# Kernel tuning notes

Measured on AMD Instinct MI355X. Metric: run time of the kernel, lower is better.

The kernel has to match this reference:

```python
import jax, jax.numpy as jnp
import numpy as np

N_HEADS = 16
LN_EPS = 1e-5

def layer_norm(x, w):
    # matches torch LayerNorm in fp32, weight-only (no bias)
    x = x.astype(jnp.float32)
    mu = jnp.mean(x, axis=-1, keepdims=True)
    var = jnp.mean((x - mu) ** 2, axis=-1, keepdims=True)
    return (x - mu) / jnp.sqrt(var + LN_EPS) * w

def rotate_half(t):
    t1, t2 = jnp.split(t, 2, axis=-1)
    return jnp.concatenate((-t2, t1), axis=-1)

def setup_inputs() -> dict:
    key = jax.random.key(0)
    ks = jax.random.split(key, 16)
    B, S, D, C = 2, 2048, 1024, 1024
    H = N_HEADS
    hd = D // H
    # rotary tables: emb = cat(freqs, freqs), freqs = t * inv_freq
    inv_freq = 1.0 / (10000.0 ** (np.arange(0, hd, 2, dtype=np.float32) / hd))
    t = np.arange(S, dtype=np.float32)
    freqs = np.outer(t, inv_freq)                       # [S, hd/2]
    emb = np.concatenate([freqs, freqs], axis=-1)       # [S, hd]
    s = 0.02
    return {
        "x": jax.random.normal(ks[0], (B, S, D), jnp.float32),
        "rotary_cos": jnp.asarray(np.cos(emb)),
        "rotary_sin": jnp.asarray(np.sin(emb)),
        "c": jax.random.normal(ks[1], (B, C), jnp.float32),
        "norm1_w": jnp.ones((D,), jnp.float32),
        "qkv_w": jax.random.normal(ks[2], (3 * D, D), jnp.float32) * s,
        "out_w": jax.random.normal(ks[3], (D, D), jnp.float32) * s,
        "norm2_w": jnp.ones((D,), jnp.float32),
        "fc1_w": jax.random.normal(ks[4], (4 * D, D), jnp.float32) * s,
        "fc1_b": jnp.zeros((4 * D,), jnp.float32),
        "fc2_w": jax.random.normal(ks[5], (D, 4 * D), jnp.float32) * s,
        "fc2_b": jnp.zeros((D,), jnp.float32),
        # NOTE: module zero-inits adaLN; random here for a non-degenerate baseline
        "ada_w": jax.random.normal(ks[6], (6 * D, C), jnp.float32) * s,
        "ada_b": jnp.zeros((6 * D,), jnp.float32),
    }

def reference(x, rotary_cos, rotary_sin, c, norm1_w, qkv_w, out_w, norm2_w,
              fc1_w, fc1_b, fc2_w, fc2_b, ada_w, ada_b):
    B, S, D = x.shape
    H = N_HEADS
    hd = D // H
    # AdaLN conditioning -> six [B,1,D] modulation tensors
    mods = (c @ ada_w.T + ada_b)[:, None, :]                       # [B,1,6D]
    shift_msa, scale_msa, gate_msa, shift_mlp, scale_mlp, gate_mlp = jnp.split(mods, 6, axis=2)
    x_skip = x
    # LN + modulate + QKV
    h = layer_norm(x, norm1_w) * (1.0 + scale_msa) + shift_msa     # [B,S,D]
    qkv = (h @ qkv_w.T).reshape(B, S, 3, H, hd)
    # rotary applied to packed qkv (q, k, and v) as in the torchscript fallback
    cos = rotary_cos[None, :, None, None, :]                       # [1,S,1,1,hd]
    sin = rotary_sin[None, :, None, None, :]
    qkv = qkv * cos + rotate_half(qkv) * sin
    q, k, v = qkv[:, :, 0], qkv[:, :, 1], qkv[:, :, 2]             # [B,S,H,hd]
    scale = hd ** -0.5
    scores = jnp.einsum('bqhd,bkhd->bhqk', q, k) * scale           # [B,H,S,S]
    attn = jax.nn.softmax(scores, axis=-1)
    o = jnp.einsum('bhqk,bkhd->bqhd', attn, v).reshape(B, S, D)
    # gated residual (dropout=0 / eval)
    x = gate_msa * (o @ out_w.T) + x_skip
    # second LN + modulate + MLP (exact gelu, matching F.gelu default)
    h2 = layer_norm(x, norm2_w) * (1.0 + scale_mlp) + shift_mlp
    mlp = jax.nn.gelu(h2 @ fc1_w.T + fc1_b, approximate=False) @ fc2_w.T + fc2_b
    return gate_mlp * mlp + x
```

## Files before the change

kernel.cpp:

```cpp
#include <hip/hip_runtime.h>
#include <hip/hip_bf16.h>


typedef unsigned short u16;
typedef unsigned int   u32;
typedef __bf16 bf16x8 __attribute__((ext_vector_type(8)));
typedef float  f32x4  __attribute__((ext_vector_type(4)));

#define MFMA_BF16(a, b, c) __builtin_amdgcn_mfma_f32_16x16x32_bf16((a), (b), (c), 0, 0, 0)

__device__ __forceinline__ float b2f(u16 u) {
    union { u32 i; float f; } v; v.i = ((u32)u) << 16; return v.f;
}
__device__ __forceinline__ u16 f2b(float f) {
    union { u32 i; float f; } v; v.f = f;
    u32 i = v.i;
    return (u16)((i + 0x7FFFu + ((i >> 16) & 1u)) >> 16);
}
__device__ __forceinline__ u32 pk2(float a, float b) {
#if __has_builtin(__builtin_amdgcn_cvt_pk_bf16_f32)
    typedef __bf16 bf16x2_t __attribute__((ext_vector_type(2)));
    union { bf16x2_t v; u32 u; } cv;
    cv.v = __builtin_amdgcn_cvt_pk_bf16_f32(a, b);
    return cv.u;
#else
    return (u32)f2b(a) | ((u32)f2b(b) << 16);
#endif
}
__device__ __forceinline__ float exp2_raw(float x) {
#if __has_builtin(__builtin_amdgcn_exp2f)
    return __builtin_amdgcn_exp2f(x);
#else
    float r;
    __asm("v_exp_f32 %0, %1" : "=v"(r) : "v"(x));
    return r;
#endif
}
__device__ __forceinline__ float finz(float v) {
    return __builtin_isfinite(v) ? v : 0.0f;
}
__device__ __forceinline__ void dma16(const void* g, void* l) {
    __builtin_amdgcn_global_load_lds(
        (const __attribute__((address_space(1))) unsigned int*)(uintptr_t)g,
        (__attribute__((address_space(3))) unsigned int*)(uintptr_t)l,
        16, 0, 0);
}

__global__ __launch_bounds__(256) void convert_kernel(
    const float* __restrict__ in, u16* __restrict__ out, int n8, int kshift)
{
    int i = blockIdx.x * 256 + threadIdx.x;
    if (i >= n8) return;
    size_t o = (size_t)i * 8;
    int bk   = (int)(o >> (kshift + 7));
    int rem  = (int)(o & (((size_t)128 << kshift) - 1));
    int kg   = rem >> 10;
    int nloc = (rem >> 3) & 127;
    const float* src = in + (((size_t)bk * 128 + nloc) << kshift) + kg * 8;
    float4 a = *(const float4*)src;
    float4 b = *(const float4*)(src + 4);
    union { u16 s[8]; float4 v; } wp;
    wp.s[0] = f2b(a.x); wp.s[1] = f2b(a.y); wp.s[2] = f2b(a.z); wp.s[3] = f2b(a.w);
    wp.s[4] = f2b(b.x); wp.s[5] = f2b(b.y); wp.s[6] = f2b(b.z); wp.s[7] = f2b(b.w);
    *(float4*)(out + o) = wp.v;
}

__global__ __launch_bounds__(64) void mods_kernel(
    const float* __restrict__ c, const float* __restrict__ ada_w,
    const float* __restrict__ ada_b, float* __restrict__ mods)
{
    const int n = blockIdx.x;
    const int lane = threadIdx.x;
    const float* wr = ada_w + (size_t)n * 1024;
    float a0 = 0.f, a1 = 0.f;
    for (int k = lane; k < 1024; k += 64) {
        float w = wr[k];
        a0 += w * c[k];
        a1 += w * c[1024 + k];
    }
    for (int o = 32; o > 0; o >>= 1) {
        a0 += __shfl_down(a0, o, 64);
        a1 += __shfl_down(a1, o, 64);
    }
    if (lane == 0) {
        float bb = ada_b[n];
        mods[n]        = a0 + bb;
        mods[6144 + n] = a1 + bb;
    }
}

__global__ __launch_bounds__(256) void ln_mod_kernel(
    const u16* __restrict__ xbf, const float* __restrict__ xf,
    const float* __restrict__ w, const float* __restrict__ mods,
    int scale_off, int shift_off, u16* __restrict__ out)
{
    const int row = blockIdx.x;
    const int b   = row >> 11;
    const int tid = threadIdx.x;
    const int wave = tid >> 6, lane = tid & 63;
    const size_t base = (size_t)row * 1024 + tid * 4;
    float v[4];
    if (xf) {
        float4 t = *(const float4*)(xf + base);
        v[0] = t.x; v[1] = t.y; v[2] = t.z; v[3] = t.w;
    } else {
        uint2 p = *(const uint2*)(xbf + base);
        union { u32 i; float f; } a, bb, cc, d;
        a.i  = p.x << 16;          v[0] = a.f;
        bb.i = p.x & 0xFFFF0000u;  v[1] = bb.f;
        cc.i = p.y << 16;          v[2] = cc.f;
        d.i  = p.y & 0xFFFF0000u;  v[3] = d.f;
    }
    float s  = v[0] + v[1] + v[2] + v[3];
    float sq = v[0]*v[0] + v[1]*v[1] + v[2]*v[2] + v[3]*v[3];
    #pragma unroll
    for (int o = 32; o > 0; o >>= 1) {
        s  += __shfl_down(s,  o, 64);
        sq += __shfl_down(sq, o, 64);
    }
    __shared__ float ws[8];
    if (lane == 0) { ws[wave] = s; ws[4 + wave] = sq; }
    __syncthreads();
    const float ts = (ws[0] + ws[1]) + (ws[2] + ws[3]);
    const float tq = (ws[4] + ws[5]) + (ws[6] + ws[7]);
    const float mean = ts * (1.0f / 1024.0f);
    const float var  = tq * (1.0f / 1024.0f) - mean * mean;
    const float inv  = rsqrtf(fmaxf(var, 0.f) + 1e-5f);
    union { u16 s4[4]; uint2 u2; } pk;
    for (int i = 0; i < 4; ++i) {
        int cidx = tid * 4 + i;
        float y = (v[i] - mean) * inv * w[cidx];
        y = y * (1.0f + mods[b * 6144 + scale_off + cidx]) + mods[b * 6144 + shift_off + cidx];
        pk.s4[i] = f2b(y);
    }
    size_t o = ((size_t)(row >> 7)) * 131072 + ((tid * 4) >> 3) * 1024
             + (row & 127) * 8 + ((tid * 4) & 7);
    *(uint2*)(out + o) = pk.u2;
}

template<int MODE, int TM>
__global__ __launch_bounds__(256) void gemm128(
    const u16* __restrict__ A, const u16* __restrict__ W,
    int M, int N, int K,
    const float* __restrict__ mods, const float* __restrict__ bias,
    const float* __restrict__ resid_f, const u16* __restrict__ resid_bf,
    float* __restrict__ out_f, u16* __restrict__ out_bf,
    u16* __restrict__ aux1, u16* __restrict__ aux2,
    const float* __restrict__ rcos, const float* __restrict__ rsin)
{
    constexpr int FI    = TM / 32;
    constexpr int WROWS = TM / 2;
    constexpr int ATILE = TM * 32;
    __shared__ u16 As[3][ATILE];
    __shared__ u16 Bs[3][4096];
    const int tid  = threadIdx.x;
    const int wave = tid >> 6, lane = tid & 63;
    const int quad = lane >> 4, l15 = lane & 15;
    const int wi = wave >> 1, wj = wave & 1;
    const int m0 = blockIdx.y * TM, n0 = blockIdx.x * 128;

    f32x4 acc[FI][4] = {};

    const u16* Asrc = A + (size_t)(m0 >> 7) * 128 * K + (m0 & 127) * 8
                        + wave * 1024 + lane * 8;
    const u16* Bsrc = W + (size_t)n0 * K + wave * 1024 + lane * 8;

    auto stage = [&](int tt, int buf) {
        const u16* a = Asrc + (size_t)tt * 4096;
        const u16* b = Bsrc + (size_t)tt * 4096;
        if constexpr (TM == 128) {
            dma16(a,       &As[buf][wave * 1024]);
            dma16(a + 512, &As[buf][wave * 1024 + 512]);
        } else {
            dma16(a, &As[buf][wave * 512]);
        }
        dma16(b,       &Bs[buf][wave * 1024]);
        dma16(b + 512, &Bs[buf][wave * 1024 + 512]);
    };

    const int nt = K >> 5;
    stage(0, 0);
    stage(1, 1);

    int cur = 0;
    for (int t = 0; t < nt; ++t) {
        if (t + 1 < nt) {
            if constexpr (TM == 128)
                __asm volatile("s_waitcnt vmcnt(4)" ::: "memory");
            else
                __asm volatile("s_waitcnt vmcnt(3)" ::: "memory");
        } else {
            __asm volatile("s_waitcnt vmcnt(0)" ::: "memory");
        }
        __builtin_amdgcn_s_barrier();
        if (t + 2 < nt) {
            int nb = cur + 2; if (nb >= 3) nb -= 3;
            stage(t + 2, nb);
        }
        bf16x8 af[FI], bw[4];
        #pragma unroll
        for (int f = 0; f < FI; ++f)
            af[f] = *(const bf16x8*)(&As[cur][quad * (TM * 8) + (wi * WROWS + f * 16 + l15) * 8]);
        #pragma unroll
        for (int f = 0; f < 4; ++f)
            bw[f] = *(const bf16x8*)(&Bs[cur][quad * 1024 + (wj * 64 + f * 16 + l15) * 8]);
        #pragma unroll
        for (int fi = 0; fi < FI; ++fi)
            #pragma unroll
            for (int fj = 0; fj < 4; ++fj)
                acc[fi][fj] = MFMA_BF16(af[fi], bw[fj], acc[fi][fj]);
        cur = (cur + 1 == 3) ? 0 : cur + 1;
    }

    if (MODE == 4) {
        const int colbase = n0 + wj * 64;
        const int wcol = colbase >> 10;
        const int hh   = (colbase & 1023) >> 6;
        #pragma unroll
        for (int fi = 0; fi < FI; ++fi) {
            const int rbase = m0 + wi * WROWS + fi * 16 + quad * 4;
            #pragma unroll
            for (int reg = 0; reg < 4; ++reg) {
                const int r = rbase + reg;
                const int b = r >> 11, s = r & 2047;
                const int bh = b * 16 + hh;
                #pragma unroll
                for (int fj = 0; fj < 2; ++fj) {
                    const int d2 = fj * 16 + l15;
                    float va = acc[fi][fj][reg];
                    float vb = acc[fi][fj + 2][reg];
                    float ca = rcos[s * 64 + d2];
                    float sa = rsin[s * 64 + d2];
                    float ra = va * ca - vb * sa;
                    float rb = vb * ca + va * sa;
                    if (wcol == 0) {
                        ra *= 0.18033688011f; rb *= 0.18033688011f;
                        u16* dst = aux1 + ((size_t)bh * 2048 + s) * 64;
                        dst[d2]      = f2b(ra);
                        dst[d2 + 32] = f2b(rb);
                    } else if (wcol == 1) {
                        size_t base = (size_t)bh * 131072 + (s >> 6) * 4096
                                    + (s & 63) * 8 + (d2 & 7);
                        aux2[base + (d2 >> 3) * 512]        = f2b(ra);
                        aux2[base + ((d2 >> 3) + 4) * 512]  = f2b(rb);
                    } else {
                        const int sl = s & 63;
                        const int sp = (sl & 32) | ((sl & 15) << 1) | ((sl >> 4) & 1);
                        size_t base = (size_t)bh * 131072 + (s >> 6) * 4096
                                    + (sp >> 3) * 512 + (sp & 7);
                        out_bf[base + d2 * 8]        = f2b(ra);
                        out_bf[base + (d2 + 32) * 8] = f2b(rb);
                    }
                }
            }
        }
        return;
    }

    #pragma unroll
    for (int fi = 0; fi < FI; ++fi) {
        #pragma unroll
        for (int fj = 0; fj < 4; ++fj) {
            const int cidx  = n0 + wj * 64 + fj * 16 + l15;
            const int rbase = m0 + wi * WROWS + fi * 16 + quad * 4;
            #pragma unroll
            for (int reg = 0; reg < 4; ++reg) {
                const int r = rbase + reg;
                float v = acc[fi][fj][reg];
                if (MODE == 1) {
                    float u = v + bias[cidx];
                    float g = 0.5f * u * (1.0f + erff(u * 0.70710678118654752f));
                    size_t o = ((size_t)(r >> 7)) * 524288 + (cidx >> 3) * 1024
                             + (r & 127) * 8 + (cidx & 7);
                    out_bf[o] = f2b(g);
                } else if (MODE == 2) {
                    int bb = r >> 11;
                    float gate = mods[bb * 6144 + 2048 + cidx];
                    out_bf[(size_t)r * N + cidx] = f2b(gate * v + resid_f[(size_t)r * N + cidx]);
                } else if (MODE == 3) {
                    int bb = r >> 11;
                    float u = v + bias[cidx];
                    float gate = mods[bb * 6144 + 5120 + cidx];
                    out_f[(size_t)r * N + cidx] =
                        finz(gate * u + b2f(resid_bf[(size_t)r * N + cidx]));
                }
            }
        }
    }
}

__global__ __launch_bounds__(256, 4) void attn_kernel(
    const u16* __restrict__ Q, const u16* __restrict__ Kb,
    const u16* __restrict__ Vb, u16* __restrict__ O)
{
    __shared__ u16 Ks[4096];
    __shared__ u16 Vs[4096];
    __shared__ u16 Ps[4][16 * 72];
    const int tid  = threadIdx.x;
    const int wave = tid >> 6, lane = tid & 63;
    const int quad = lane >> 4, l15 = lane & 15;
    const int bh = blockIdx.x & 31, qt = blockIdx.x >> 5;

    const u16* Qh = Q + ((size_t)bh * 2048 + qt * 64) * 64;

    const int soff = (2 * wave) * 512 + lane * 8;
    const u16* kSrc = Kb + (size_t)bh * 131072 + soff;
    const u16* vSrc = Vb + (size_t)bh * 131072 + soff;
    u16* kDst0 = &Ks[(2 * wave) * 512];
    u16* kDst1 = &Ks[(2 * wave + 1) * 512];
    u16* vDst0 = &Vs[(2 * wave) * 512];
    u16* vDst1 = &Vs[(2 * wave + 1) * 512];

    bf16x8 aq[2];
    #pragma unroll
    for (int kh = 0; kh < 2; ++kh)
        aq[kh] = *(const bf16x8*)(Qh + (size_t)(wave * 16 + l15) * 64 + kh * 32 + quad * 8);

    f32x4 acc_o[4] = {};
    float lsum[4] = {0.f, 0.f, 0.f, 0.f};

    for (int kb = 0; kb < 32; ++kb) {
        __syncthreads();
        dma16(kSrc,       kDst0);
        dma16(kSrc + 512, kDst1);
        dma16(vSrc,       vDst0);
        dma16(vSrc + 512, vDst1);
        kSrc += 4096; vSrc += 4096;
        __syncthreads();

        f32x4 sc[4] = {};
        #pragma unroll
        for (int kt = 0; kt < 4; ++kt)
            #pragma unroll
            for (int kh = 0; kh < 2; ++kh) {
                bf16x8 bk = *(const bf16x8*)(&Ks[(quad + kh * 4) * 512 + (kt * 16 + l15) * 8]);
                sc[kt] = MFMA_BF16(aq[kh], bk, sc[kt]);
            }

        #pragma unroll
        for (int kt = 0; kt < 4; ++kt)
            #pragma unroll
            for (int reg = 0; reg < 4; ++reg)
                sc[kt][reg] = exp2_raw(fminf(sc[kt][reg], 72.f));
        #pragma unroll
        for (int reg = 0; reg < 4; ++reg)
            lsum[reg] += (sc[0][reg] + sc[1][reg]) + (sc[2][reg] + sc[3][reg]);

        #pragma unroll
        for (int reg = 0; reg < 4; ++reg) {
            u32* prow = (u32*)(&Ps[wave][(quad * 4 + reg) * 72]);
            prow[l15]      = pk2(sc[0][reg], sc[1][reg]);
            prow[16 + l15] = pk2(sc[2][reg], sc[3][reg]);
        }
        __asm volatile("s_waitcnt lgkmcnt(0)" ::: "memory");

        bf16x8 ap0 = *(const bf16x8*)(&Ps[wave][l15 * 72 + quad * 8]);
        bf16x8 ap1 = *(const bf16x8*)(&Ps[wave][l15 * 72 + 32 + quad * 8]);
        #pragma unroll
        for (int dt = 0; dt < 4; ++dt) {
            bf16x8 bv0 = *(const bf16x8*)(&Vs[quad * 512 + (dt * 16 + l15) * 8]);
            bf16x8 bv1 = *(const bf16x8*)(&Vs[(quad + 4) * 512 + (dt * 16 + l15) * 8]);
            acc_o[dt] = MFMA_BF16(ap0, bv0, acc_o[dt]);
            acc_o[dt] = MFMA_BF16(ap1, bv1, acc_o[dt]);
        }
    }

    float linv[4];
    #pragma unroll
    for (int reg = 0; reg < 4; ++reg) {
        float l = lsum[reg];
        l += __shfl_xor(l, 1, 64);
        l += __shfl_xor(l, 2, 64);
        l += __shfl_xor(l, 4, 64);
        l += __shfl_xor(l, 8, 64);
        linv[reg] = 1.0f / l;
    }

    const int b = bh >> 4, hh = bh & 15;
    #pragma unroll
    for (int dt = 0; dt < 4; ++dt)
        #pragma unroll
        for (int reg = 0; reg < 4; ++reg) {
            int q = qt * 64 + wave * 16 + quad * 4 + reg;
            int r = b * 2048 + q;
            int col = hh * 64 + dt * 16 + l15;
            float v = acc_o[dt][reg] * linv[reg];
            O[((size_t)(r >> 7)) * 131072 + (col >> 3) * 1024
              + (r & 127) * 8 + (col & 7)] = f2b(v);
        }
}

extern "C" void kernel_launch(void* const* d_in, const int* in_sizes, int n_in,
                              void* d_out, int out_size, void* d_ws, size_t ws_size,
                              hipStream_t stream)
{
    const float* x     = (const float*)d_in[0];
    const float* rcos  = (const float*)d_in[1];
    const float* rsin  = (const float*)d_in[2];
    const float* c     = (const float*)d_in[3];
    const float* n1w   = (const float*)d_in[4];
    const float* qkvw  = (const float*)d_in[5];
    const float* outw  = (const float*)d_in[6];
    const float* n2w   = (const float*)d_in[7];
    const float* fc1w  = (const float*)d_in[8];
    const float* fc1b  = (const float*)d_in[9];
    const float* fc2w  = (const float*)d_in[10];
    const float* fc2b  = (const float*)d_in[11];
    const float* adaw  = (const float*)d_in[12];
    const float* adab  = (const float*)d_in[13];
    float* out = (float*)d_out;

    char* ws = (char*)d_ws;
    const size_t MB8 = (size_t)8 * 1024 * 1024;
    float* mods  = (float*)ws;
    u16*   W     = (u16*)(ws + 49152);
    char*  S1    = ws + 49152 + MB8;
    char*  S2    = S1 + MB8;

    u16* h    = (u16*)d_out;
    u16* qs   = (u16*)S1;
    u16* ks   = (u16*)S2;
    u16* vT   = (u16*)(S2 + MB8);
    u16* ob   = (u16*)d_out;
    u16* x2   = (u16*)S1;
    u16* h2   = (u16*)d_out;
    u16* mid  = (u16*)S2;

    mods_kernel<<<6144, 64, 0, stream>>>(c, adaw, adab, mods);
    ln_mod_kernel<<<4096, 256, 0, stream>>>(nullptr, x, n1w, mods, 1024, 0, h);
    convert_kernel<<<1536, 256, 0, stream>>>(qkvw, W, 393216, 10);
    gemm128<4, 128><<<dim3(24, 32), 256, 0, stream>>>(h, W, 4096, 3072, 1024,
        nullptr, nullptr, nullptr, nullptr, nullptr, vT, qs, ks, rcos, rsin);
    attn_kernel<<<1024, 256, 0, stream>>>(qs, ks, vT, ob);
    convert_kernel<<<512, 256, 0, stream>>>(outw, W, 131072, 10);
    gemm128<2, 64><<<dim3(8, 64), 256, 0, stream>>>(ob, W, 4096, 1024, 1024,
        mods, nullptr, x, nullptr, nullptr, x2, nullptr, nullptr, nullptr, nullptr);
    ln_mod_kernel<<<4096, 256, 0, stream>>>(x2, nullptr, n2w, mods, 4096, 3072, h2);
    convert_kernel<<<2048, 256, 0, stream>>>(fc1w, W, 524288, 10);
    gemm128<1, 128><<<dim3(32, 32), 256, 0, stream>>>(h2, W, 4096, 4096, 1024,
        nullptr, fc1b, nullptr, nullptr, nullptr, mid, nullptr, nullptr, nullptr, nullptr);
    convert_kernel<<<2048, 256, 0, stream>>>(fc2w, W, 524288, 12);
    gemm128<3, 64><<<dim3(8, 64), 256, 0, stream>>>(mid, W, 4096, 1024, 4096,
        mods, fc2b, nullptr, x2, out, nullptr, nullptr, nullptr, nullptr, nullptr);
}
```

Measured before the change: 384.0 us.

## Double attention query tile to 128 rows and merge QKV/out weight conversions

```diff
diff --git a/kernel.cpp b/kernel.cpp
--- a/kernel.cpp
+++ b/kernel.cpp
@@ -46,11 +46,9 @@
         16, 0, 0);
 }
 
-__global__ __launch_bounds__(256) void convert_kernel(
-    const float* __restrict__ in, u16* __restrict__ out, int n8, int kshift)
-{
-    int i = blockIdx.x * 256 + threadIdx.x;
-    if (i >= n8) return;
+__device__ __forceinline__ void convert_body(
+    const float* __restrict__ in, u16* __restrict__ out, int i, int kshift)
+{
     size_t o = (size_t)i * 8;
     int bk   = (int)(o >> (kshift + 7));
     int rem  = (int)(o & (((size_t)128 << kshift) - 1));
@@ -63,6 +61,27 @@
     wp.s[0] = f2b(a.x); wp.s[1] = f2b(a.y); wp.s[2] = f2b(a.z); wp.s[3] = f2b(a.w);
     wp.s[4] = f2b(b.x); wp.s[5] = f2b(b.y); wp.s[6] = f2b(b.z); wp.s[7] = f2b(b.w);
     *(float4*)(out + o) = wp.v;
+}
+
+__global__ __launch_bounds__(256) void convert_kernel(
+    const float* __restrict__ in, u16* __restrict__ out, int n8, int kshift)
+{
+    int i = blockIdx.x * 256 + threadIdx.x;
+    if (i >= n8) return;
+    convert_body(in, out, i, kshift);
+}
+
+__global__ __launch_bounds__(256) void convert2_kernel(
+    const float* __restrict__ in0, u16* __restrict__ out0, int n80,
+    const float* __restrict__ in1, u16* __restrict__ out1, int n81)
+{
+    int i = blockIdx.x * 256 + threadIdx.x;
+    if (i < n80) {
+        convert_body(in0, out0, i, 10);
+    } else {
+        i -= n80;
+        if (i < n81) convert_body(in1, out1, i, 10);
+    }
 }
 
 __global__ __launch_bounds__(64) void mods_kernel(
@@ -289,27 +308,25 @@
     }
 }
 
-__global__ __launch_bounds__(256, 4) void attn_kernel(
+__global__ __launch_bounds__(512, 2) void attn_kernel(
     const u16* __restrict__ Q, const u16* __restrict__ Kb,
     const u16* __restrict__ Vb, u16* __restrict__ O)
 {
     __shared__ u16 Ks[4096];
     __shared__ u16 Vs[4096];
-    __shared__ u16 Ps[4][16 * 72];
+    __shared__ u16 Ps[8][16 * 72];
     const int tid  = threadIdx.x;
     const int wave = tid >> 6, lane = tid & 63;
     const int quad = lane >> 4, l15 = lane & 15;
     const int bh = blockIdx.x & 31, qt = blockIdx.x >> 5;
 
-    const u16* Qh = Q + ((size_t)bh * 2048 + qt * 64) * 64;
-
-    const int soff = (2 * wave) * 512 + lane * 8;
+    const u16* Qh = Q + ((size_t)bh * 2048 + qt * 128) * 64;
+
+    const int soff = wave * 512 + lane * 8;
     const u16* kSrc = Kb + (size_t)bh * 131072 + soff;
     const u16* vSrc = Vb + (size_t)bh * 131072 + soff;
-    u16* kDst0 = &Ks[(2 * wave) * 512];
-    u16* kDst1 = &Ks[(2 * wave + 1) * 512];
-    u16* vDst0 = &Vs[(2 * wave) * 512];
-    u16* vDst1 = &Vs[(2 * wave + 1) * 512];
+    u16* kDst = &Ks[wave * 512];
+    u16* vDst = &Vs[wave * 512];
 
     bf16x8 aq[2];
     #pragma unroll
@@ -321,10 +338,8 @@
 
     for (int kb = 0; kb < 32; ++kb) {
         __syncthreads();
-        dma16(kSrc,       kDst0);
-        dma16(kSrc + 512, kDst1);
-        dma16(vSrc,       vDst0);
-        dma16(vSrc + 512, vDst1);
+        dma16(kSrc, kDst);
+        dma16(vSrc, vDst);
         kSrc += 4096; vSrc += 4096;
         __syncthreads();
 
@@ -381,7 +396,7 @@
     for (int dt = 0; dt < 4; ++dt)
         #pragma unroll
         for (int reg = 0; reg < 4; ++reg) {
-            int q = qt * 64 + wave * 16 + quad * 4 + reg;
+            int q = qt * 128 + wave * 16 + quad * 4 + reg;
             int r = b * 2048 + q;
             int col = hh * 64 + dt * 16 + l15;
             float v = acc_o[dt][reg] * linv[reg];
@@ -425,15 +440,15 @@
     u16* x2   = (u16*)S1;
     u16* h2   = (u16*)d_out;
     u16* mid  = (u16*)S2;
+    u16* Wo   = W + 3145728;
 
     mods_kernel<<<6144, 64, 0, stream>>>(c, adaw, adab, mods);
     ln_mod_kernel<<<4096, 256, 0, stream>>>(nullptr, x, n1w, mods, 1024, 0, h);
-    convert_kernel<<<1536, 256, 0, stream>>>(qkvw, W, 393216, 10);
+    convert2_kernel<<<2048, 256, 0, stream>>>(qkvw, W, 393216, outw, Wo, 131072);
     gemm128<4, 128><<<dim3(24, 32), 256, 0, stream>>>(h, W, 4096, 3072, 1024,
         nullptr, nullptr, nullptr, nullptr, nullptr, vT, qs, ks, rcos, rsin);
-    attn_kernel<<<1024, 256, 0, stream>>>(qs, ks, vT, ob);
-    convert_kernel<<<512, 256, 0, stream>>>(outw, W, 131072, 10);
-    gemm128<2, 64><<<dim3(8, 64), 256, 0, stream>>>(ob, W, 4096, 1024, 1024,
+    attn_kernel<<<512, 512, 0, stream>>>(qs, ks, vT, ob);
+    gemm128<2, 64><<<dim3(8, 64), 256, 0, stream>>>(ob, Wo, 4096, 1024, 1024,
         mods, nullptr, x, nullptr, nullptr, x2, nullptr, nullptr, nullptr, nullptr);
     ln_mod_kernel<<<4096, 256, 0, stream>>>(x2, nullptr, n2w, mods, 4096, 3072, h2);
     convert_kernel<<<2048, 256, 0, stream>>>(fc1w, W, 524288, 10);
```

After: 412.2 us. +7.4%, slower.
